# Performance work log

Measured on AMD Instinct MI355X. Metric: run time of the kernel, lower is better.

Reference implementation:

```python
import jax, jax.numpy as jnp
import numpy as np

N = 20000      # nodes (drugs, scaled to production size)
E = 640000     # edges
R = 65         # relation types
F_IN = 128     # input feature dim (trimnet embedding)
H1 = 64        # hidden1
H2 = 32        # hidden2 (bilinear discriminator dim)
B = 8192       # drug pairs in idx


def setup_inputs() -> dict:
    key = jax.random.key(0)
    ks = jax.random.split(key, 20)
    s = 0.05
    return {
        "x_o": jax.random.normal(ks[0], (N, F_IN), jnp.float32),
        "x_a": jax.random.normal(ks[1], (N, F_IN), jnp.float32),
        "features1": jax.random.normal(ks[2], (N, F_IN), jnp.float32),
        "W1": jax.random.normal(ks[3], (R, F_IN, H1), jnp.float32) * s,
        "root1": jax.random.normal(ks[4], (F_IN, H1), jnp.float32) * s,
        "b1": jnp.zeros((H1,), jnp.float32),
        "W2": jax.random.normal(ks[5], (R, H1, H2), jnp.float32) * s,
        "root2": jax.random.normal(ks[6], (H1, H2), jnp.float32) * s,
        "b2": jnp.zeros((H2,), jnp.float32),
        "attt": jnp.array([0.5, 0.5], jnp.float32),
        "disc_W": jax.random.normal(ks[7], (H2, H2), jnp.float32) * s,
        "disc_b": jnp.zeros((), jnp.float32),
        "cls_W": jax.random.normal(ks[8], (448, R), jnp.float32) * s,
        "cls_b": jnp.zeros((R,), jnp.float32),
        "edge_index": jax.random.randint(ks[9], (2, E), 0, N, jnp.int32),
        "e_type": jax.random.randint(ks[10], (E,), 0, R, jnp.int32),
        "e_type1": jax.random.randint(ks[11], (E,), 0, R, jnp.int32),
        "idx": jax.random.randint(ks[12], (2, B), 0, N, jnp.int32),
    }


def rgcn(x, src, dst, etype, W, root, b):
    """RGCNConv with per-relation mean aggregation (PyG default aggr='mean').
    Aggregates source features per (relation, dst) via one segment_sum, then
    applies the relation weights once with a batched matmul."""
    n, fin = x.shape
    seg = etype * n + dst                       # combined (relation, dst) segment id
    msg = x[src]                                # [E, fin] gather
    agg = jax.ops.segment_sum(msg, seg, num_segments=R * n).reshape(R, n, fin)
    cnt = jax.ops.segment_sum(jnp.ones((src.shape[0],), x.dtype), seg,
                              num_segments=R * n).reshape(R, n, 1)
    agg = agg / jnp.maximum(cnt, 1.0)           # per-relation mean
    out = jnp.einsum('rnf,rfh->nh', agg, W)     # sum over relations of W_r @ mean_r
    return out + x @ root + b


def reference(x_o, x_a, features1, W1, root1, b1, W2, root2, b2, attt,
              disc_W, disc_b, cls_W, cls_b, edge_index, e_type, e_type1, idx):
    src, dst = edge_index[0], edge_index[1]

    def enc(x, et):
        h1 = jax.nn.relu(rgcn(x, src, dst, et, W1, root1, b1))
        # dropout is identity in eval mode
        h2 = rgcn(h1, src, dst, et, W2, root2, b2)
        return h1, h2

    x1_o, x2_o = enc(x_o, e_type)
    _, x2_o_a = enc(x_a, e_type)
    _, x2_o_a_a = enc(x_o, e_type1)

    c = jax.nn.sigmoid(jnp.mean(x2_o, axis=0))  # readout + sigmoid, [H2]

    def disc(h_pl, h_mi):
        s1 = h_pl @ disc_W @ c + disc_b         # bilinear f_k(h, c)
        s2 = h_mi @ disc_W @ c + disc_b
        return jnp.stack([s1, s2], axis=1)      # [N, 2]

    ret_os = disc(x2_o, x2_o_a)
    ret_os_a = disc(x2_o, x2_o_a_a)

    final = jnp.concatenate([attt[0] * x1_o, attt[1] * x2_o], axis=1)  # [N, 96]
    e1 = jnp.concatenate([final[idx[0]], features1[idx[0]]], axis=1)   # [B, 224]
    e2 = jnp.concatenate([final[idx[1]], features1[idx[1]]], axis=1)
    log = jnp.concatenate([e1, e2], axis=1) @ cls_W + cls_b            # [B, 65]
    return (log, ret_os, ret_os_a, x2_o)
```

## Files before the change

### kernel.cpp

```cpp
#include <hip/hip_runtime.h>
#include <hip/hip_bf16.h>

#define NN 20000
#define EE 640000
#define RR 65
#define FIN1 128
#define HH1 64
#define HH2 32
#define BB 8192

constexpr int BM = 128;
constexpr int NBH = 256;
constexpr int GRID_PRE = 2048;
constexpr int EPB = EE / NBH;
constexpr int NBT = (NN + BM - 1) / BM;
constexpr int NOCT = 8;
constexpr int NPO = NN / NOCT;
constexpr int NB2 = NOCT * RR;
constexpr int MAXT2 = EE / BM + NB2;

constexpr int CLS_K  = 512;
constexpr int CLS_N  = 80;
constexpr int CLS_CK = 128;
constexpr int CLS_BM = 64;

typedef __attribute__((ext_vector_type(8))) short short8;
typedef __attribute__((ext_vector_type(4))) float floatx4;
typedef __attribute__((ext_vector_type(4))) unsigned int uint4e;
typedef __attribute__((ext_vector_type(2))) unsigned int uint2e;

constexpr size_t aln(size_t x) { return (x + 255) & ~(size_t)255; }

constexpr size_t OFF_CSUM  = 0;
constexpr size_t OFF_CNTD  = aln(OFF_CSUM + 32 * 4);
constexpr size_t ZERO_BYTES = OFF_CNTD + (size_t)NN * 4;
constexpr size_t OFF_DSTOFF = aln(ZERO_BYTES);
constexpr size_t OFF_BH0   = aln(OFF_DSTOFF + ((size_t)NN + 1) * 4);
constexpr size_t OFF_BH1   = OFF_BH0 + (size_t)NBH * NB2 * 4;
constexpr size_t OFF_BB0   = OFF_BH1 + (size_t)NBH * NB2 * 4;
constexpr size_t OFF_BB1   = OFF_BB0 + (size_t)NBH * NB2 * 4;
constexpr size_t OFF_HT    = aln(OFF_BB1 + (size_t)NBH * NB2 * 4);
constexpr size_t OFF_OFFB0 = aln(OFF_HT + (size_t)2 * NB2 * 4);
constexpr size_t OFF_OFFB1 = OFF_OFFB0 + (NB2 + 1) * 4;
constexpr size_t OFF_TILB0 = aln(OFF_OFFB1 + (NB2 + 1) * 4);
constexpr size_t OFF_TILT0 = OFF_TILB0 + (size_t)MAXT2 * 4;
constexpr size_t OFF_TILB1 = OFF_TILT0 + (size_t)MAXT2 * 4;
constexpr size_t OFF_TILT1 = OFF_TILB1 + (size_t)MAXT2 * 4;
constexpr size_t OFF_SLOT  = aln(OFF_TILT1 + (size_t)MAXT2 * 4);
constexpr size_t OFF_POSD  = OFF_SLOT + (size_t)EE * 4;
constexpr size_t OFF_RDP   = OFF_POSD + (size_t)EE * 4;
constexpr size_t OFF_WD0   = OFF_RDP + (size_t)EE * 4;
constexpr size_t OFF_WD1   = OFF_WD0 + (size_t)EE * 4;
constexpr size_t OFF_PERM0 = OFF_WD1 + (size_t)EE * 4;
constexpr size_t OFF_PERM1 = OFF_PERM0 + (size_t)EE * 4;
constexpr size_t OFF_XOB   = aln(OFF_PERM1 + (size_t)EE * 4);
constexpr size_t OFF_XAB   = OFF_XOB + (size_t)NN * FIN1 * 2;
constexpr size_t OFF_H1    = aln(OFF_XAB + (size_t)NN * FIN1 * 2);
constexpr size_t OFF_H1B   = OFF_H1 + (size_t)3 * NN * HH1 * 4;
constexpr size_t OFF_X2A   = OFF_H1B + (size_t)3 * NN * HH1 * 2;
constexpr size_t OFF_X2AA  = OFF_X2A + (size_t)NN * HH2 * 4;
constexpr size_t OFF_W1BT  = OFF_X2AA + (size_t)NN * HH2 * 4;
constexpr size_t OFF_W2BT  = OFF_W1BT + (size_t)RR * HH1 * FIN1 * 2;
constexpr size_t OFF_R1T   = OFF_W2BT + (size_t)RR * HH2 * HH1 * 2;
constexpr size_t OFF_R2T   = OFF_R1T + (size_t)HH1 * FIN1 * 2;
constexpr size_t OFF_CWT   = OFF_R2T + (size_t)HH2 * HH1 * 2;
constexpr size_t OFF_PART  = aln(OFF_CWT + (size_t)CLS_N * CLS_K * 2);
constexpr size_t OFF_MSG   = aln(OFF_PART + (size_t)256 * 32 * 4);
constexpr size_t MSG_B1    = (size_t)EE * HH1 * 2;
constexpr size_t MSG_B2    = (size_t)EE * HH2 * 2;
constexpr size_t WS_END    = OFF_MSG + MSG_B1;

constexpr size_t O_LOG  = 0;
constexpr size_t O_ROS  = (size_t)BB * RR;
constexpr size_t O_ROSA = O_ROS + (size_t)NN * 2;
constexpr size_t O_X2O  = O_ROSA + (size_t)NN * 2;

__device__ inline unsigned short f2bf(float f) {
    __hip_bfloat16 h = __float2bfloat16(f);
    return *reinterpret_cast<unsigned short*>(&h);
}
__device__ inline float bfbits2f(unsigned int hi_bits) {
    return __uint_as_float(hi_bits);
}

struct GemmEnc {
    const unsigned short* X;
    unsigned short* msg;
    const unsigned int* perm;
    const int* offB;
    const int* tilB;
    const int* tilT;
};
struct GemmArgs { GemmEnc e[3]; };

struct RedEnc {
    const unsigned short* msg;
    const float* wD;
    float* base;
    unsigned short* bfout;
};
struct RedArgs { RedEnc e[3]; };

__global__ void k_hist(const int* __restrict__ ei, const int* __restrict__ et0,
                       const int* __restrict__ et1,
                       int* cntD, int* __restrict__ slotE,
                       int* __restrict__ bh0, int* __restrict__ bh1,
                       const float* __restrict__ x_o, const float* __restrict__ x_a,
                       const float* __restrict__ W1, const float* __restrict__ W2,
                       const float* __restrict__ root1, const float* __restrict__ root2,
                       const float* __restrict__ clsW,
                       unsigned short* xob, unsigned short* xab,
                       unsigned short* w1t, unsigned short* w2t,
                       unsigned short* r1t, unsigned short* r2t,
                       unsigned short* cwt) {
    __shared__ int lh0[NB2], lh1[NB2];
    int t = threadIdx.x;
    if (blockIdx.x < NBH) {
        for (int p = t; p < NB2; p += 256) { lh0[p] = 0; lh1[p] = 0; }
        __syncthreads();
        int base = blockIdx.x * EPB;
        for (int i = t; i < EPB; i += 256) {
            int e = base + i;
            int oct = ei[e] / NPO;
            atomicAdd(&lh0[oct * RR + et0[e]], 1);
            atomicAdd(&lh1[oct * RR + et1[e]], 1);
            slotE[e] = atomicAdd(&cntD[ei[EE + e]], 1);
        }
        __syncthreads();
        for (int p = t; p < NB2; p += 256) {
            bh0[blockIdx.x * NB2 + p] = lh0[p];
            bh1[blockIdx.x * NB2 + p] = lh1[p];
        }
    }
    int stride = gridDim.x * 256;
    int i0 = blockIdx.x * 256 + t;
    const int NX4 = NN * FIN1 / 4;
    const float4* xo4 = (const float4*)x_o;
    const float4* xa4 = (const float4*)x_a;
    for (int i = i0; i < NX4; i += stride) {
        float4 a = xo4[i], b = xa4[i];
        uint2 pa, pb;
        pa.x = (unsigned)f2bf(a.x) | ((unsigned)f2bf(a.y) << 16);
        pa.y = (unsigned)f2bf(a.z) | ((unsigned)f2bf(a.w) << 16);
        pb.x = (unsigned)f2bf(b.x) | ((unsigned)f2bf(b.y) << 16);
        pb.y = (unsigned)f2bf(b.z) | ((unsigned)f2bf(b.w) << 16);
        ((uint2*)xob)[i] = pa;
        ((uint2*)xab)[i] = pb;
    }
    const int NW1_4 = RR * HH1 * FIN1 / 4;
    for (int i4 = i0; i4 < NW1_4; i4 += stride) {
        int i = i4 * 4;
        int k = i % FIN1; int rh = i / FIN1; int hh = rh % HH1; int r = rh / HH1;
        const float* s = &W1[((size_t)r * FIN1 + k) * HH1 + hh];
        uint2 pk;
        pk.x = (unsigned)f2bf(s[0]) | ((unsigned)f2bf(s[HH1]) << 16);
        pk.y = (unsigned)f2bf(s[2 * HH1]) | ((unsigned)f2bf(s[3 * HH1]) << 16);
        ((uint2*)w1t)[i4] = pk;
    }
    const int NW2_4 = RR * HH2 * HH1 / 4;
    for (int i4 = i0; i4 < NW2_4; i4 += stride) {
        int i = i4 * 4;
        int k = i % HH1; int rh = i / HH1; int hh = rh % HH2; int r = rh / HH2;
        const float* s = &W2[((size_t)r * HH1 + k) * HH2 + hh];
        uint2 pk;
        pk.x = (unsigned)f2bf(s[0]) | ((unsigned)f2bf(s[HH2]) << 16);
        pk.y = (unsigned)f2bf(s[2 * HH2]) | ((unsigned)f2bf(s[3 * HH2]) << 16);
        ((uint2*)w2t)[i4] = pk;
    }
    const int NR1_4 = HH1 * FIN1 / 4;
    for (int i4 = i0; i4 < NR1_4; i4 += stride) {
        int i = i4 * 4;
        int k = i % FIN1; int hh = i / FIN1;
        const float* s = &root1[(size_t)k * HH1 + hh];
        uint2 pk;
        pk.x = (unsigned)f2bf(s[0]) | ((unsigned)f2bf(s[HH1]) << 16);
        pk.y = (unsigned)f2bf(s[2 * HH1]) | ((unsigned)f2bf(s[3 * HH1]) << 16);
        ((uint2*)r1t)[i4] = pk;
    }
    const int NR2_4 = HH2 * HH1 / 4;
    for (int i4 = i0; i4 < NR2_4; i4 += stride) {
        int i = i4 * 4;
        int k = i % HH1; int hh = i / HH1;
        const float* s = &root2[(size_t)k * HH2 + hh];
        uint2 pk;
        pk.x = (unsigned)f2bf(s[0]) | ((unsigned)f2bf(s[HH2]) << 16);
        pk.y = (unsigned)f2bf(s[2 * HH2]) | ((unsigned)f2bf(s[3 * HH2]) << 16);
        ((uint2*)r2t)[i4] = pk;
    }
    const int NCW_4 = CLS_N * CLS_K / 4;
    for (int i4 = i0; i4 < NCW_4; i4 += stride) {
        int i = i4 * 4;
        int k = i % CLS_K; int n = i / CLS_K;
        uint2 pk = {0u, 0u};
        if (n < RR && k < 448) {
            const float* s = &clsW[(size_t)k * RR + n];
            pk.x = (unsigned)f2bf(s[0]) | ((unsigned)f2bf(s[RR]) << 16);
            pk.y = (unsigned)f2bf(s[2 * RR]) | ((unsigned)f2bf(s[3 * RR]) << 16);
        }
        ((uint2*)cwt)[i4] = pk;
    }
}

__global__ void k_scanD(const int* __restrict__ cntD, int* __restrict__ dstOff) {
    __shared__ int s[256];
    int t = threadIdx.x;
    constexpr int PER = (NN + 255) / 256;
    int lo = t * PER, hi = min(NN, lo + PER);
    int sum = 0;
    for (int i = lo; i < hi; i++) sum += cntD[i];
    s[t] = sum;
    __syncthreads();
    for (int ofs = 1; ofs < 256; ofs <<= 1) {
        int v = 0;
        if (t >= ofs) v = s[t - ofs];
        __syncthreads();
        if (t >= ofs) s[t] += v;
        __syncthreads();
    }
    int run = s[t] - sum;
    for (int i = lo; i < hi; i++) { dstOff[i] = run; run += cntD[i]; }
    if (t == 255) dstOff[NN] = run;
}

__global__ void k_post(const int* __restrict__ ei, const int* __restrict__ et0,
                       const int* __restrict__ et1, const int* __restrict__ dstOff,
                       const int* __restrict__ slotE,
                       int* __restrict__ posD, unsigned int* __restrict__ rdP) {
    int e = blockIdx.x * 256 + threadIdx.x;
    if (e < EE) {
        int d = ei[EE + e];
        int pos = dstOff[d] + slotE[e];
        posD[e] = pos;
        rdP[pos] = (unsigned)et0[e] | ((unsigned)et1[e] << 16);
    }
}

__global__ void k_scanB1(const int* __restrict__ bh0, const int* __restrict__ bh1,
                         int* __restrict__ bb0, int* __restrict__ bb1,
                         int* __restrict__ hT) {
    int w = (blockIdx.x * 256 + threadIdx.x) >> 6;
    int lane = threadIdx.x & 63;
    if (w >= 2 * NB2) return;
    int s = w / NB2, k = w % NB2;
    const int* bh = s ? bh1 : bh0;
    int* bb = s ? bb1 : bb0;
    int v[4];
    #pragma unroll
    for (int i = 0; i < 4; i++) v[i] = bh[(size_t)(lane * 4 + i) * NB2 + k];
    int ls = v[0] + v[1] + v[2] + v[3];
    int inc = ls;
    #pragma unroll
    for (int ofs = 1; ofs < 64; ofs <<= 1) {
        int o = __shfl_up(inc, ofs);
        if (lane >= ofs) inc += o;
    }
    int run = inc - ls;
    #pragma unroll
    for (int i = 0; i < 4; i++) {
        bb[(size_t)(lane * 4 + i) * NB2 + k] = run;
        run += v[i];
    }
    if (lane == 63) hT[s * NB2 + k] = run;
}

__global__ void k_scanB2(const int* __restrict__ hT,
                         int* offB0, int* offB1,
                         int* tilB0, int* tilT0, int* tilB1, int* tilT1) {
    __shared__ int h[2][NB2];
    __shared__ int o[2][NB2 + 1];
    __shared__ int to[2][NB2 + 1];
    __shared__ int csumE[2][8], csumT[2][8];
    int t = threadIdx.x;
    for (int p = t; p < 2 * NB2; p += 256) h[p / NB2][p % NB2] = hT[p];
    __syncthreads();
    if (t < 16) {
        int s = t / 8, c = t % 8;
        int runE = 0, runT = 0;
        for (int k = c * RR; k < (c + 1) * RR; k++) {
            o[s][k] = runE;  runE += h[s][k];
            to[s][k] = runT; runT += (h[s][k] + BM - 1) / BM;
        }
        csumE[s][c] = runE; csumT[s][c] = runT;
    }
    __syncthreads();
    if (t < 2) {
        int runE = 0, runT = 0;
        for (int c = 0; c < 8; c++) {
            int e = csumE[t][c], tt = csumT[t][c];
            csumE[t][c] = runE; csumT[t][c] = runT;
            runE += e; runT += tt;
        }
        o[t][NB2] = runE; to[t][NB2] = runT;
    }
    __syncthreads();
    if (t < 16) {
        int s = t / 8, c = t % 8;
        for (int k = c * RR; k < (c + 1) * RR; k++) {
            o[s][k] += csumE[s][c];
            to[s][k] += csumT[s][c];
        }
    }
    __syncthreads();
    for (int p = t; p <= NB2; p += 256) { offB0[p] = o[0][p]; offB1[p] = o[1][p]; }
    for (int i = t; i < MAXT2; i += 256) {
        #pragma unroll
        for (int s = 0; s < 2; s++) {
            int total = to[s][NB2];
            int bkt = -1, ti = 0;
            if (i < total) {
                int lo = 0, hi = NB2;
                while (hi - lo > 1) { int mid = (lo + hi) >> 1; if (to[s][mid] <= i) lo = mid; else hi = mid; }
                bkt = lo;
                ti = i - to[s][lo];
            }
            if (s == 0) { tilB0[i] = bkt; tilT0[i] = ti; }
            else        { tilB1[i] = bkt; tilT1[i] = ti; }
        }
    }
}

__global__ void k_fillB(const int* __restrict__ ei, const int* __restrict__ et0,
                        const int* __restrict__ et1, const int* __restrict__ posD,
                        const int* __restrict__ offB0, const int* __restrict__ offB1,
                        const int* __restrict__ bb0, const int* __restrict__ bb1,
                        unsigned int* perm0, unsigned int* perm1) {
    __shared__ int lc[2][NB2];
    __shared__ int lb[2][NB2];
    int t = threadIdx.x;
    for (int p = t; p < NB2; p += 256) {
        lc[0][p] = 0; lc[1][p] = 0;
        lb[0][p] = offB0[p] + bb0[blockIdx.x * NB2 + p];
        lb[1][p] = offB1[p] + bb1[blockIdx.x * NB2 + p];
    }
    __syncthreads();
    int base = blockIdx.x * EPB;
    for (int i = t; i < EPB; i += 256) {
        int e = base + i;
        int src = ei[e];
        int pos = posD[e];
        int oct = src / NPO;
        unsigned int packed = ((unsigned)(src - oct * NPO) << 20) | (unsigned)pos;
        int k0 = oct * RR + et0[e];
        int k1 = oct * RR + et1[e];
        int p0 = atomicAdd(&lc[0][k0], 1);
        int p1 = atomicAdd(&lc[1][k1], 1);
        perm0[lb[0][k0] + p0] = packed;
        perm1[lb[1][k1] + p1] = packed;
    }
}

__global__ void k_wts(const int* __restrict__ dstOff, const unsigned int* __restrict__ rdP,
                      float* __restrict__ wD0, float* __restrict__ wD1) {
    constexpr int CAP = 96;
    __shared__ unsigned int ld[4][CAP];
    int wave = threadIdx.x >> 6;
    int lane = threadIdx.x & 63;
    int d = blockIdx.x * 4 + wave;
    int j0 = 0, deg = 0;
    if (d < NN) { j0 = dstOff[d]; deg = dstOff[d + 1] - j0; }
    for (int j = lane; j < deg && j < CAP; j += 64) ld[wave][j] = rdP[j0 + j];
    __syncthreads();
    for (int j = lane; j < deg; j += 64) {
        unsigned int my = (j < CAP) ? ld[wave][j] : rdP[j0 + j];
        unsigned int m0 = my & 0xffffu, m1 = my >> 16;
        int c0 = 0, c1 = 0;
        for (int k = 0; k < deg; k++) {
            unsigned int p = (k < CAP) ? ld[wave][k] : rdP[j0 + k];
            c0 += ((p & 0xffffu) == m0);
            c1 += ((p >> 16) == m1);
        }
        wD0[j0 + j] = 1.0f / (float)c0;
        wD1[j0 + j] = 1.0f / (float)c1;
    }
}

template <int FIN, int HOUT>
__launch_bounds__(256, 3)
__global__ void k_bgemm(const unsigned short* __restrict__ X0,
                        const unsigned short* __restrict__ X1,
                        const unsigned short* __restrict__ X2,
                        const unsigned short* __restrict__ rootT,
                        const float* __restrict__ bias,
                        float* O0, float* O1, float* O2) {
    const int enc = blockIdx.y;
    const unsigned short* X = enc == 0 ? X0 : enc == 1 ? X1 : X2;
    float* O = enc == 0 ? O0 : enc == 1 ? O1 : O2;
    int n0 = blockIdx.x * BM;
    int mcount = min(BM, NN - n0);

    constexpr int LDK = FIN + 8;
    __shared__ unsigned short As[BM][LDK];
    __shared__ unsigned short Bs[HOUT][LDK];

    int tid = threadIdx.x;
    {
        constexpr int CHB = HOUT * FIN / 8;
        for (int c = tid; c < CHB; c += 256) {
            int row = c / (FIN / 8), cc = c % (FIN / 8);
            *(uint4*)&Bs[row][cc * 8] = *(const uint4*)&rootT[row * FIN + cc * 8];
        }
    }
    {
        constexpr int CHA = BM * FIN / 8;
        for (int c = tid; c < CHA; c += 256) {
            int row = c / (FIN / 8), cc = c % (FIN / 8);
            uint4 v = {0u, 0u, 0u, 0u};
            if (row < mcount) v = *(const uint4*)&X[(size_t)(n0 + row) * FIN + cc * 8];
            *(uint4*)&As[row][cc * 8] = v;
        }
    }
    __syncthreads();

    const int wave = tid >> 6;
    const int lane = tid & 63;
    const int q = lane >> 4;
    const int ln = lane & 15;
    constexpr int NT = HOUT / 16;
    constexpr int KS = FIN / 32;
    const int mbase = wave * 32;

    floatx4 acc[2][NT];
    #pragma unroll
    for (int a = 0; a < 2; a++)
        #pragma unroll
        for (int nt = 0; nt < NT; nt++) acc[a][nt] = floatx4{0.f, 0.f, 0.f, 0.f};

    for (int ks = 0; ks < KS; ks++) {
        int kk = ks * 32 + q * 8;
        short8 af0 = *(const short8*)&As[mbase + ln][kk];
        short8 af1 = *(const short8*)&As[mbase + 16 + ln][kk];
        #pragma unroll
        for (int nt = 0; nt < NT; nt++) {
            short8 bf = *(const short8*)&Bs[nt * 16 + ln][kk];
            acc[0][nt] = __builtin_amdgcn_mfma_f32_16x16x32_bf16(af0, bf, acc[0][nt], 0, 0, 0);
            acc[1][nt] = __builtin_amdgcn_mfma_f32_16x16x32_bf16(af1, bf, acc[1][nt], 0, 0, 0);
        }
    }

    #pragma unroll
    for (int mt = 0; mt < 2; mt++) {
        #pragma unroll
        for (int rr2 = 0; rr2 < 4; rr2++) {
            int i = mbase + mt * 16 + q * 4 + rr2;
            int n = n0 + i;
            if (i < mcount) {
                #pragma unroll
                for (int nt = 0; nt < NT; nt++)
                    O[(size_t)n * HOUT + nt * 16 + ln] = acc[mt][nt][rr2] + bias[nt * 16 + ln];
            }
        }
    }
}

template <int FIN, int HOUT>
__launch_bounds__(256, (FIN == 128 ? 3 : 4))
__global__ void k_gemm(GemmArgs ga, const unsigned short* __restrict__ WT) {
    const GemmEnc ge = ga.e[blockIdx.y];
    int b = blockIdx.x;
    int bkt = ge.tilB[b];
    if (bkt < 0) return;
    int r = bkt % RR;
    int srcBase = (bkt / RR) * NPO;
    int t = ge.tilT[b];
    int ebase = ge.offB[bkt] + t * BM;
    int mcount = min(BM, ge.offB[bkt + 1] - ebase);

    constexpr int LDK = FIN + 8;
    __shared__ unsigned short As[BM][LDK];
    __shared__ unsigned short Bs[HOUT][LDK];
    __shared__ int Sr[BM];
    __shared__ int Pd[BM];

    int tid = threadIdx.x;
    if (tid < BM) {
        if (tid < mcount) {
            unsigned int p = ge.perm[ebase + tid];
            Sr[tid] = srcBase + (int)(p >> 20);
            Pd[tid] = (int)(p & 0xFFFFFu);
        } else { Sr[tid] = -1; Pd[tid] = 0; }
    }
    __syncthreads();

    {
        const unsigned short* Wr = WT + (size_t)r * HOUT * FIN;
        constexpr int CHB = HOUT * FIN / 8;
        for (int c = tid; c < CHB; c += 256) {
            int row = c / (FIN / 8), cc = c % (FIN / 8);
            *(uint4*)&Bs[row][cc * 8] = *(const uint4*)&Wr[row * FIN + cc * 8];
        }
    }
    {
        constexpr int CHA = BM * FIN / 8;
        for (int c = tid; c < CHA; c += 256) {
            int row = c / (FIN / 8), cc = c % (FIN / 8);
            int s = Sr[row];
            uint4 v = {0u, 0u, 0u, 0u};
            if (s >= 0) v = *(const uint4*)&ge.X[(size_t)s * FIN + cc * 8];
            *(uint4*)&As[row][cc * 8] = v;
        }
    }
    __syncthreads();

    const int wave = tid >> 6;
    const int lane = tid & 63;
    const int q = lane >> 4;
    const int ln = lane & 15;
    constexpr int NT = HOUT / 16;
    constexpr int KS = FIN / 32;
    const int mbase = wave * 32;

    floatx4 acc[2][NT];
    #pragma unroll
    for (int a = 0; a < 2; a++)
        #pragma unroll
        for (int nt = 0; nt < NT; nt++) acc[a][nt] = floatx4{0.f, 0.f, 0.f, 0.f};

    for (int ks = 0; ks < KS; ks++) {
        int kk = ks * 32 + q * 8;
        short8 af0 = *(const short8*)&As[mbase + ln][kk];
        short8 af1 = *(const short8*)&As[mbase + 16 + ln][kk];
        #pragma unroll
        for (int nt = 0; nt < NT; nt++) {
            short8 bf = *(const short8*)&Bs[nt * 16 + ln][kk];
            acc[0][nt] = __builtin_amdgcn_mfma_f32_16x16x32_bf16(af0, bf, acc[0][nt], 0, 0, 0);
            acc[1][nt] = __builtin_amdgcn_mfma_f32_16x16x32_bf16(af1, bf, acc[1][nt], 0, 0, 0);
        }
    }

    __syncthreads();
    constexpr int LDM = HOUT + 8;
    unsigned short* Ms = &As[0][0];
    #pragma unroll
    for (int mt = 0; mt < 2; mt++) {
        #pragma unroll
        for (int rr2 = 0; rr2 < 4; rr2++) {
            int i = mbase + mt * 16 + q * 4 + rr2;
            #pragma unroll
            for (int nt = 0; nt < NT; nt++)
                Ms[i * LDM + nt * 16 + ln] = f2bf(acc[mt][nt][rr2]);
        }
    }
    __syncthreads();
    constexpr int CH = HOUT / 8;
    for (int c = tid; c < BM * CH; c += 256) {
        int row = c / CH, cc = c % CH;
        if (row < mcount) {
            uint4e v = *(const uint4e*)&Ms[row * LDM + cc * 8];
            *(uint4e*)&ge.msg[(size_t)Pd[row] * HOUT + cc * 8] = v;
        }
    }
}

template <int H, bool RELU>
__global__ void k_reduce(RedArgs ra, const int* __restrict__ dstOff) {
    const RedEnc re = ra.e[blockIdx.y];
    int d = blockIdx.x * 4 + (threadIdx.x >> 6);
    if (d >= NN) return;
    int lane = threadIdx.x & 63;
    constexpr int HC = H / 4;
    constexpr int RPI = 64 / HC;
    int sub = lane / HC;
    int c4 = lane % HC;
    int j0 = dstOff[d], j1 = dstOff[d + 1];
    double a0 = 0.0, a1 = 0.0, a2 = 0.0, a3 = 0.0;
    for (int j = j0 + sub; j < j1; j += RPI) {
        float w = re.wD[j];
        uint2e v = *(const uint2e*)&re.msg[(size_t)j * H + c4 * 4];
        a0 += (double)(w * bfbits2f(v.x << 16));
        a1 += (double)(w * bfbits2f(v.x & 0xffff0000u));
        a2 += (double)(w * bfbits2f(v.y << 16));
        a3 += (double)(w * bfbits2f(v.y & 0xffff0000u));
    }
    #pragma unroll
    for (int ofs = 32; ofs >= HC; ofs >>= 1) {
        a0 += __shfl_down(a0, ofs); a1 += __shfl_down(a1, ofs);
        a2 += __shfl_down(a2, ofs); a3 += __shfl_down(a3, ofs);
    }
    if (lane < HC) {
        size_t o = (size_t)d * H + c4 * 4;
        float v0 = re.base[o] + (float)a0, v1 = re.base[o + 1] + (float)a1;
        float v2 = re.base[o + 2] + (float)a2, v3 = re.base[o + 3] + (float)a3;
        if (RELU) {
            v0 = fmaxf(v0, 0.f); v1 = fmaxf(v1, 0.f);
            v2 = fmaxf(v2, 0.f); v3 = fmaxf(v3, 0.f);
        }
        re.base[o] = v0; re.base[o + 1] = v1; re.base[o + 2] = v2; re.base[o + 3] = v3;
        if (RELU) {
            re.bfout[o] = f2bf(v0); re.bfout[o + 1] = f2bf(v1);
            re.bfout[o + 2] = f2bf(v2); re.bfout[o + 3] = f2bf(v3);
        }
    }
}

__global__ void k_mean(const float* __restrict__ x2o, float* __restrict__ part) {
    __shared__ float s[256];
    int t = threadIdx.x; int hh = t & 31; int g = t >> 5;
    float acc = 0.f;
    for (int n = blockIdx.x * 8 + g; n < NN; n += gridDim.x * 8)
        acc += x2o[(size_t)n * 32 + hh];
    s[t] = acc;
    __syncthreads();
    if (t < 32) {
        float v = 0.f;
        for (int gg = 0; gg < 8; gg++) v += s[gg * 32 + t];
        part[blockIdx.x * 32 + t] = v;
    }
}

__global__ void k_csum(const float* __restrict__ part, float* __restrict__ csum) {
    int t = threadIdx.x;
    if (t < 32) {
        double a = 0.0;
        for (int b = 0; b < 256; b++) a += (double)part[b * 32 + t];
        csum[t] = (float)a;
    }
}

__global__ void k_disc(const float* __restrict__ x2o, const float* __restrict__ x2a,
                       const float* __restrict__ x2aa, const float* __restrict__ csum,
                       const float* __restrict__ discW, const float* __restrict__ discb,
                       float* ret_os, float* ret_osa) {
    __shared__ float c[32], v[32];
    int t = threadIdx.x;
    if (t < 32) c[t] = 1.f / (1.f + expf(-csum[t] * (1.f / NN)));
    __syncthreads();
    if (t < 32) {
        float a = 0.f;
        for (int j = 0; j < 32; j++) a += discW[t * 32 + j] * c[j];
        v[t] = a;
    }
    __syncthreads();
    float db = discb[0];
    int n = blockIdx.x * 256 + t;
    if (n < NN) {
        float s1 = 0.f, s2 = 0.f, s3 = 0.f;
        for (int j = 0; j < 32; j++) {
            float vj = v[j];
            s1 += x2o[(size_t)n * 32 + j] * vj;
            s2 += x2a[(size_t)n * 32 + j] * vj;
            s3 += x2aa[(size_t)n * 32 + j] * vj;
        }
        ret_os[n * 2] = s1 + db;  ret_os[n * 2 + 1] = s2 + db;
        ret_osa[n * 2] = s1 + db; ret_osa[n * 2 + 1] = s3 + db;
    }
}

__launch_bounds__(256, 2)
__global__ void k_clsg(const float* __restrict__ h1o, const float* __restrict__ x2o,
                       const float* __restrict__ feat, const float* __restrict__ attt,
                       const int* __restrict__ idx,
                       const unsigned short* __restrict__ cwt,
                       const float* __restrict__ clsb, float* __restrict__ log_out) {
    constexpr int LDK = CLS_CK + 8;
    __shared__ unsigned short As[CLS_BM][LDK];
    __shared__ unsigned short Bs[CLS_N][LDK];
    __shared__ int nd[2][CLS_BM];

    int tid = threadIdx.x;
    int p0 = blockIdx.x * CLS_BM;
    if (tid < CLS_BM) {
        nd[0][tid] = idx[p0 + tid];
        nd[1][tid] = idx[BB + p0 + tid];
    }
    float a0 = attt[0], a1 = attt[1];

    const int wave = tid >> 6;
    const int lane = tid & 63;
    const int q = lane >> 4;
    const int ln = lane & 15;
    constexpr int NT = CLS_N / 16;
    const int mbase = wave * 16;

    floatx4 acc[NT];
    #pragma unroll
    for (int nt = 0; nt < NT; nt++) acc[nt] = floatx4{0.f, 0.f, 0.f, 0.f};

    for (int ch = 0; ch < CLS_K / CLS_CK; ch++) {
        int kbase = ch * CLS_CK;
        __syncthreads();
        for (int c = tid; c < CLS_N * CLS_CK / 8; c += 256) {
            int row = c / (CLS_CK / 8), cc = c % (CLS_CK / 8);
            *(uint4*)&Bs[row][cc * 8] = *(const uint4*)&cwt[(size_t)row * CLS_K + kbase + cc * 8];
        }
        for (int c = tid; c < CLS_BM * CLS_CK / 4; c += 256) {
            int row = c / (CLS_CK / 4);
            int j4 = (c % (CLS_CK / 4)) * 4;
            int j = kbase + j4;
            float4 v = {0.f, 0.f, 0.f, 0.f};
            if (j < 448) {
                int hseg = j / 224, jj = j % 224;
                int node = nd[hseg][row];
                if (jj < 64) {
                    v = *(const float4*)&h1o[(size_t)node * 64 + jj];
                    v.x *= a0; v.y *= a0; v.z *= a0; v.w *= a0;
                } else if (jj < 96) {
                    v = *(const float4*)&x2o[(size_t)node * 32 + (jj - 64)];
                    v.x *= a1; v.y *= a1; v.z *= a1; v.w *= a1;
                } else {
                    v = *(const float4*)&feat[(size_t)node * 128 + (jj - 96)];
                }
            }
            uint2 pk;
            pk.x = (unsigned)f2bf(v.x) | ((unsigned)f2bf(v.y) << 16);
            pk.y = (unsigned)f2bf(v.z) | ((unsigned)f2bf(v.w) << 16);
            *(uint2*)&As[row][j4] = pk;
        }
        __syncthreads();
        #pragma unroll
        for (int ks = 0; ks < CLS_CK / 32; ks++) {
            int kk = ks * 32 + q * 8;
            short8 af = *(const short8*)&As[mbase + ln][kk];
            #pragma unroll
            for (int nt = 0; nt < NT; nt++) {
                short8 bf = *(const short8*)&Bs[nt * 16 + ln][kk];
                acc[nt] = __builtin_amdgcn_mfma_f32_16x16x32_bf16(af, bf, acc[nt], 0, 0, 0);
            }
        }
    }

    #pragma unroll
    for (int rr2 = 0; rr2 < 4; rr2++) {
        int i = mbase + q * 4 + rr2;
        int pair = p0 + i;
        #pragma unroll
        for (int nt = 0; nt < NT; nt++) {
            int col = nt * 16 + ln;
            if (col < RR)
                log_out[(size_t)pair * RR + col] = acc[nt][rr2] + clsb[col];
        }
    }
}

extern "C" void kernel_launch(void* const* d_in, const int* in_sizes, int n_in,
                              void* d_out, int out_size, void* d_ws, size_t ws_size,
                              hipStream_t stream) {
    const float* x_o   = (const float*)d_in[0];
    const float* x_a   = (const float*)d_in[1];
    const float* feat  = (const float*)d_in[2];
    const float* W1    = (const float*)d_in[3];
    const float* root1 = (const float*)d_in[4];
    const float* b1    = (const float*)d_in[5];
    const float* W2    = (const float*)d_in[6];
    const float* root2 = (const float*)d_in[7];
    const float* b2    = (const float*)d_in[8];
    const float* attt  = (const float*)d_in[9];
    const float* discW = (const float*)d_in[10];
    const float* discb = (const float*)d_in[11];
    const float* clsW  = (const float*)d_in[12];
    const float* clsb  = (const float*)d_in[13];
    const int* ei      = (const int*)d_in[14];
    const int* et0     = (const int*)d_in[15];
    const int* et1     = (const int*)d_in[16];
    const int* idx     = (const int*)d_in[17];

    char* ws = (char*)d_ws;
    float* csum = (float*)(ws + OFF_CSUM);
    int* cntD  = (int*)(ws + OFF_CNTD);
    int* dstOff = (int*)(ws + OFF_DSTOFF);
    int* bh0   = (int*)(ws + OFF_BH0);
    int* bh1   = (int*)(ws + OFF_BH1);
    int* bb0   = (int*)(ws + OFF_BB0);
    int* bb1   = (int*)(ws + OFF_BB1);
    int* hT    = (int*)(ws + OFF_HT);
    int* offB0 = (int*)(ws + OFF_OFFB0);
    int* offB1 = (int*)(ws + OFF_OFFB1);
    int* tilB0 = (int*)(ws + OFF_TILB0);
    int* tilT0 = (int*)(ws + OFF_TILT0);
    int* tilB1 = (int*)(ws + OFF_TILB1);
    int* tilT1 = (int*)(ws + OFF_TILT1);
    int* slotE = (int*)(ws + OFF_SLOT);
    int* posD  = (int*)(ws + OFF_POSD);
    unsigned int* rdP = (unsigned int*)(ws + OFF_RDP);
    float* wD0 = (float*)(ws + OFF_WD0);
    float* wD1 = (float*)(ws + OFF_WD1);
    unsigned int* perm0 = (unsigned int*)(ws + OFF_PERM0);
    unsigned int* perm1 = (unsigned int*)(ws + OFF_PERM1);
    unsigned short* xob = (unsigned short*)(ws + OFF_XOB);
    unsigned short* xab = (unsigned short*)(ws + OFF_XAB);
    float* h1o  = (float*)(ws + OFF_H1);
    float* h1a  = h1o + (size_t)NN * HH1;
    float* h1aa = h1a + (size_t)NN * HH1;
    unsigned short* h1bo  = (unsigned short*)(ws + OFF_H1B);
    unsigned short* h1ba  = h1bo + (size_t)NN * HH1;
    unsigned short* h1baa = h1ba + (size_t)NN * HH1;
    float* x2a  = (float*)(ws + OFF_X2A);
    float* x2aa = (float*)(ws + OFF_X2AA);
    unsigned short* w1t = (unsigned short*)(ws + OFF_W1BT);
    unsigned short* w2t = (unsigned short*)(ws + OFF_W2BT);
    unsigned short* r1t = (unsigned short*)(ws + OFF_R1T);
    unsigned short* r2t = (unsigned short*)(ws + OFF_R2T);
    unsigned short* cwt = (unsigned short*)(ws + OFF_CWT);
    float* part = (float*)(ws + OFF_PART);
    unsigned short* msg = (unsigned short*)(ws + OFF_MSG);

    float* out = (float*)d_out;
    float* log_out = out + O_LOG;
    float* ret_os  = out + O_ROS;
    float* ret_osa = out + O_ROSA;
    float* x2o     = out + O_X2O;

    size_t availMsg = ws_size > OFF_MSG ? ws_size - OFF_MSG : MSG_B1;
    int nb1 = (availMsg >= 2 * MSG_B1) ? 2 : 1;
    int nb2 = (availMsg >= 3 * MSG_B2) ? 3 : (availMsg >= 2 * MSG_B2 ? 2 : 1);

    hipMemsetAsync(ws, 0, ZERO_BYTES, stream);

    k_hist<<<GRID_PRE, 256, 0, stream>>>(ei, et0, et1, cntD, slotE, bh0, bh1,
                                         x_o, x_a, W1, W2, root1, root2, clsW,
                                         xob, xab, w1t, w2t, r1t, r2t, cwt);
    k_scanD<<<1, 256, 0, stream>>>(cntD, dstOff);
    k_post<<<2500, 256, 0, stream>>>(ei, et0, et1, dstOff, slotE, posD, rdP);
    k_scanB1<<<(2 * NB2 + 3) / 4, 256, 0, stream>>>(bh0, bh1, bb0, bb1, hT);
    k_scanB2<<<1, 256, 0, stream>>>(hT, offB0, offB1,
                                    tilB0, tilT0, tilB1, tilT1);
    k_fillB<<<NBH, 256, 0, stream>>>(ei, et0, et1, posD, offB0, offB1, bb0, bb1,
                                     perm0, perm1);
    k_wts<<<NN / 4, 256, 0, stream>>>(dstOff, rdP, wD0, wD1);

    {
        dim3 gb(NBT, 3);
        k_bgemm<FIN1, HH1><<<gb, 256, 0, stream>>>(xob, xab, xob, r1t, b1,
                                                   h1o, h1a, h1aa);
        const unsigned short* Xs[3] = {xob, xab, xob};
        float* Os[3] = {h1o, h1a, h1aa};
        unsigned short* Obs[3] = {h1bo, h1ba, h1baa};
        for (int e0 = 0; e0 < 3; ) {
            int g = 3 - e0 < nb1 ? 3 - e0 : nb1;
            GemmArgs ga{};
            RedArgs ra{};
            for (int j = 0; j < g; j++) {
                int enc = e0 + j;
                unsigned short* mb = msg + (size_t)j * EE * HH1;
                ga.e[j].X    = Xs[enc];
                ga.e[j].msg  = mb;
                ga.e[j].perm = enc == 2 ? perm1 : perm0;
                ga.e[j].offB = enc == 2 ? offB1 : offB0;
                ga.e[j].tilB = enc == 2 ? tilB1 : tilB0;
                ga.e[j].tilT = enc == 2 ? tilT1 : tilT0;
                ra.e[j].msg  = mb;
                ra.e[j].wD   = enc == 2 ? wD1 : wD0;
                ra.e[j].base = Os[enc];
                ra.e[j].bfout = Obs[enc];
            }
            k_gemm<FIN1, HH1><<<dim3(MAXT2, g), 256, 0, stream>>>(ga, w1t);
            k_reduce<HH1, true><<<dim3(NN / 4, g), 256, 0, stream>>>(ra, dstOff);
            e0 += g;
        }
    }

    {
        dim3 gb(NBT, 3);
        k_bgemm<HH1, HH2><<<gb, 256, 0, stream>>>(h1bo, h1ba, h1baa, r2t, b2,
                                                  x2o, x2a, x2aa);
        const unsigned short* Xs[3] = {h1bo, h1ba, h1baa};
        float* Os[3] = {x2o, x2a, x2aa};
        for (int e0 = 0; e0 < 3; ) {
            int g = 3 - e0 < nb2 ? 3 - e0 : nb2;
            GemmArgs ga{};
            RedArgs ra{};
            for (int j = 0; j < g; j++) {
                int enc = e0 + j;
                unsigned short* mb = msg + (size_t)j * EE * HH2;
                ga.e[j].X    = Xs[enc];
                ga.e[j].msg  = mb;
                ga.e[j].perm = enc == 2 ? perm1 : perm0;
                ga.e[j].offB = enc == 2 ? offB1 : offB0;
                ga.e[j].tilB = enc == 2 ? tilB1 : tilB0;
                ga.e[j].tilT = enc == 2 ? tilT1 : tilT0;
                ra.e[j].msg  = mb;
                ra.e[j].wD   = enc == 2 ? wD1 : wD0;
                ra.e[j].base = Os[enc];
                ra.e[j].bfout = nullptr;
            }
            k_gemm<HH1, HH2><<<dim3(MAXT2, g), 256, 0, stream>>>(ga, w2t);
            k_reduce<HH2, false><<<dim3(NN / 4, g), 256, 0, stream>>>(ra, dstOff);
            e0 += g;
        }
    }

    k_mean<<<256, 256, 0, stream>>>(x2o, part);
    k_csum<<<1, 64, 0, stream>>>(part, csum);
    k_disc<<<(NN + 255) / 256, 256, 0, stream>>>(x2o, x2a, x2aa, csum, discW, discb,
                                                 ret_os, ret_osa);
    k_clsg<<<BB / CLS_BM, 256, 0, stream>>>(h1o, x2o, feat, attt, idx, cwt, clsb, log_out);
}
```

Baseline: 595.3 us.

## Load GEMM operands directly from global into registers, dropping LDS staging

The per-relation edge GEMM kernel no longer stages gathered source rows and relation weights in shared memory. Each wave loads its MFMA A fragments straight from global into registers and reads weight fragments from global/cache per MFMA, and the bf16 outputs are written straight to the message buffer with 2-byte scattered stores instead of through an LDS transpose. Raising the occupancy hint in launch bounds is meant to hide the extra global latency. The risks are uncoalesced narrow stores, redundant weight loads across waves, and register pressure under the tighter bound.

```diff
diff --git a/kernel.cpp b/kernel.cpp
--- a/kernel.cpp
+++ b/kernel.cpp
@@ -453,7 +453,7 @@
 }
 
 template <int FIN, int HOUT>
-__launch_bounds__(256, (FIN == 128 ? 3 : 4))
+__launch_bounds__(256, (FIN == 128 ? 5 : 6))
 __global__ void k_gemm(GemmArgs ga, const unsigned short* __restrict__ WT) {
     const GemmEnc ge = ga.e[blockIdx.y];
     int b = blockIdx.x;
@@ -465,9 +465,6 @@
     int ebase = ge.offB[bkt] + t * BM;
     int mcount = min(BM, ge.offB[bkt + 1] - ebase);
 
-    constexpr int LDK = FIN + 8;
-    __shared__ unsigned short As[BM][LDK];
-    __shared__ unsigned short Bs[HOUT][LDK];
     __shared__ int Sr[BM];
     __shared__ int Pd[BM];
 
@@ -477,27 +474,7 @@
             unsigned int p = ge.perm[ebase + tid];
             Sr[tid] = srcBase + (int)(p >> 20);
             Pd[tid] = (int)(p & 0xFFFFFu);
-        } else { Sr[tid] = -1; Pd[tid] = 0; }
-    }
-    __syncthreads();
-
-    {
-        const unsigned short* Wr = WT + (size_t)r * HOUT * FIN;
-        constexpr int CHB = HOUT * FIN / 8;
-        for (int c = tid; c < CHB; c += 256) {
-            int row = c / (FIN / 8), cc = c % (FIN / 8);
-            *(uint4*)&Bs[row][cc * 8] = *(const uint4*)&Wr[row * FIN + cc * 8];
-        }
-    }
-    {
-        constexpr int CHA = BM * FIN / 8;
-        for (int c = tid; c < CHA; c += 256) {
-            int row = c / (FIN / 8), cc = c % (FIN / 8);
-            int s = Sr[row];
-            uint4 v = {0u, 0u, 0u, 0u};
-            if (s >= 0) v = *(const uint4*)&ge.X[(size_t)s * FIN + cc * 8];
-            *(uint4*)&As[row][cc * 8] = v;
-        }
+        } else { Sr[tid] = srcBase; Pd[tid] = 0; }
     }
     __syncthreads();
 
@@ -509,44 +486,44 @@
     constexpr int KS = FIN / 32;
     const int mbase = wave * 32;
 
+    const unsigned short* a0p = ge.X + (size_t)Sr[mbase + ln] * FIN + q * 8;
+    const unsigned short* a1p = ge.X + (size_t)Sr[mbase + 16 + ln] * FIN + q * 8;
+    const unsigned short* bp  = WT + (size_t)r * HOUT * FIN + (size_t)ln * FIN + q * 8;
+
+    short8 A0[KS], A1[KS];
+    #pragma unroll
+    for (int ks = 0; ks < KS; ks++) {
+        A0[ks] = *(const short8*)(a0p + ks * 32);
+        A1[ks] = *(const short8*)(a1p + ks * 32);
+    }
+
     floatx4 acc[2][NT];
     #pragma unroll
     for (int a = 0; a < 2; a++)
         #pragma unroll
         for (int nt = 0; nt < NT; nt++) acc[a][nt] = floatx4{0.f, 0.f, 0.f, 0.f};
 
-    for (int ks = 0; ks < KS; ks++) {
-        int kk = ks * 32 + q * 8;
-        short8 af0 = *(const short8*)&As[mbase + ln][kk];
-        short8 af1 = *(const short8*)&As[mbase + 16 + ln][kk];
+    #pragma unroll
+    for (int nt = 0; nt < NT; nt++) {
         #pragma unroll
-        for (int nt = 0; nt < NT; nt++) {
-            short8 bf = *(const short8*)&Bs[nt * 16 + ln][kk];
-            acc[0][nt] = __builtin_amdgcn_mfma_f32_16x16x32_bf16(af0, bf, acc[0][nt], 0, 0, 0);
-            acc[1][nt] = __builtin_amdgcn_mfma_f32_16x16x32_bf16(af1, bf, acc[1][nt], 0, 0, 0);
-        }
-    }
-
-    __syncthreads();
-    constexpr int LDM = HOUT + 8;
-    unsigned short* Ms = &As[0][0];
+        for (int ks = 0; ks < KS; ks++) {
+            short8 bf = *(const short8*)(bp + (size_t)nt * 16 * FIN + ks * 32);
+            acc[0][nt] = __builtin_amdgcn_mfma_f32_16x16x32_bf16(A0[ks], bf, acc[0][nt], 0, 0, 0);
+            acc[1][nt] = __builtin_amdgcn_mfma_f32_16x16x32_bf16(A1[ks], bf, acc[1][nt], 0, 0, 0);
+        }
+    }
+
     #pragma unroll
     for (int mt = 0; mt < 2; mt++) {
         #pragma unroll
         for (int rr2 = 0; rr2 < 4; rr2++) {
             int i = mbase + mt * 16 + q * 4 + rr2;
-            #pragma unroll
-            for (int nt = 0; nt < NT; nt++)
-                Ms[i * LDM + nt * 16 + ln] = f2bf(acc[mt][nt][rr2]);
-        }
-    }
-    __syncthreads();
-    constexpr int CH = HOUT / 8;
-    for (int c = tid; c < BM * CH; c += 256) {
-        int row = c / CH, cc = c % CH;
-        if (row < mcount) {
-            uint4e v = *(const uint4e*)&Ms[row * LDM + cc * 8];
-            *(uint4e*)&ge.msg[(size_t)Pd[row] * HOUT + cc * 8] = v;
+            if (i < mcount) {
+                unsigned short* mrow = ge.msg + (size_t)Pd[i] * HOUT + ln;
+                #pragma unroll
+                for (int nt = 0; nt < NT; nt++)
+                    mrow[nt * 16] = f2bf(acc[mt][nt][rr2]);
+            }
         }
     }
 }
```

Measured after the change: 671.3 us. 12.8% more time.
